# Optimization experiments

Hardware: AMD Instinct MI355X
Metric: run time of the kernel (lower is better)

The kernel has to match this reference:

```python
import jax, jax.numpy as jnp
import numpy as np

H, D, KV, S, PAST, BS, NB = 32, 128, 8, 128, 8064, 128, 128
T = PAST + S          # total context = 8192
NBLK = T // BS        # logical blocks used = 64
NEG = jnp.float32(-1e30)


def setup_inputs() -> dict:
    key = jax.random.key(0)
    ks = jax.random.split(key, 6)
    q = jax.random.normal(ks[0], (1, H, S, D), jnp.float32)
    k = jax.random.normal(ks[1], (1, KV, S, D), jnp.float32)
    v = jax.random.normal(ks[2], (1, KV, S, D), jnp.float32)
    pk = jax.random.normal(ks[3], (NB, KV, BS, D), jnp.float32)
    pv = jax.random.normal(ks[4], (NB, KV, BS, D), jnp.float32)
    # block table: 64 logical blocks mapped to distinct physical blocks (paged indirection)
    bt = jax.random.permutation(ks[5], NB)[:NBLK].astype(jnp.int32)
    return dict(
        query_state=q, key_state=k, value_state=v,
        attn_mask=jnp.ones((1,), jnp.float32),  # unused: causal prefill path (use_attention_mask=False)
        past_key_state=pk, past_value_state=pv,
        seq_position=PAST,
        scale=jnp.float32(1.0 / np.sqrt(D)),
        block_tables=bt, block_size=BS,
    )


def reference(query_state, key_state, value_state, attn_mask,
              past_key_state, past_value_state, seq_position, scale,
              block_tables, block_size):
    # phase == 'prefill', use_attention_mask=False -> paged_causal_attn_prefill
    kvh = past_key_state.shape[1]
    s_new = query_state.shape[2]
    total = seq_position + s_new  # static python int

    # --- append new K/V into the paged cache at positions [seq_position, total) ---
    pos_new = seq_position + jnp.arange(s_new)
    blk = block_tables[pos_new // block_size]
    off = pos_new % block_size
    k_new = jnp.transpose(key_state[0], (1, 0, 2))    # [S, KV, D]
    v_new = jnp.transpose(value_state[0], (1, 0, 2))
    kc = past_key_state.at[blk, :, off, :].set(k_new)
    vc = past_value_state.at[blk, :, off, :].set(v_new)

    # --- gather the full context [0, total) through the block table ---
    pos = jnp.arange(total)
    blk_a = block_tables[pos // block_size]
    off_a = pos % block_size
    K = kc[blk_a, :, off_a, :]   # [T, KV, D]
    V = vc[blk_a, :, off_a, :]

    # --- grouped-query causal attention ---
    g = query_state.shape[1] // kvh
    q = query_state.reshape(kvh, g, s_new, -1)                 # [KV, G, S, D]
    scores = jnp.einsum('kgsd,tkd->kgst', q, K) * scale        # [KV, G, S, T]
    causal = pos[None, :] <= (seq_position + jnp.arange(s_new))[:, None]  # [S, T]
    scores = jnp.where(causal[None, None], scores, NEG)
    probs = jax.nn.softmax(scores, axis=-1)
    out = jnp.einsum('kgst,tkd->kgsd', probs, V)               # [KV, G, S, D]

    h = kvh * g
    out = out.reshape(1, h, s_new, -1)                         # [1, H, S, D]
    out = jnp.transpose(out, (0, 2, 1, 3)).reshape(1, s_new, h * out.shape[-1])
    return out
```

## Files before the change

kernel.cpp:

```cpp
#include <hip/hip_runtime.h>
#include <hip/hip_bf16.h>


typedef unsigned short u16;
typedef unsigned int u32;
typedef __bf16 bf16x8 __attribute__((ext_vector_type(8)));
typedef float f32x16 __attribute__((ext_vector_type(16)));
typedef float f32x4 __attribute__((ext_vector_type(4)));
typedef u32 u32x4 __attribute__((ext_vector_type(4)));
typedef u32 u32x2 __attribute__((ext_vector_type(2)));

#define NHEAD 32
#define DH 128
#define NKV 8
#define SQ 128
#define PAST_T 8064
#define TOTAL_T 8192
#define BK 32
#define KSTR 136
#define VSTR 34
#define WSPP (16384 + 256)
#define MSUB 17.3123405f

__device__ __forceinline__ u32 pk2f(float lo, float hi) {
  union {
    __hip_bfloat162 b;
    u32 u;
  } cv;
  cv.b = __float22bfloat162_rn(make_float2(lo, hi));
  return cv.u;
}

template <int NPART>
__global__ __launch_bounds__(512, 1) void flash_part(
    const float* __restrict__ q, const float* __restrict__ knew,
    const float* __restrict__ vnew, const float* __restrict__ pk,
    const float* __restrict__ pv, const int* __restrict__ btab,
    const float* __restrict__ scp, float* __restrict__ ws) {
  constexpr int CHUNK = TOTAL_T / NPART;
  constexpr int NITER = CHUNK / BK;
  __shared__ __attribute__((aligned(16))) u16 k_s[2 * BK * KSTR];
  __shared__ __attribute__((aligned(16))) u16 vt_s[2 * DH * VSTR];
  __shared__ int bt_s[64];

  const int bid = blockIdx.x;
  const int kv = bid & 7;
  const int t = bid >> 3;
  const int p = t % NPART;
  const int gp = t / NPART;

  const int tid = threadIdx.x;
  const int wid = tid >> 6;
  const int lane = tid & 63;
  const int g2 = wid & 1;
  const int w = wid >> 1;
  const int h = kv * 4 + gp * 2 + g2;
  const int l31 = lane & 31, grp = lane >> 5;
  const int pstart = p * CHUNK;

  if (tid < 64) bt_s[tid] = btab[tid];
  const float qs = scp[0] * 1.44269504f;

  u32x4 qf[8];
  {
    const float* qp = q + ((size_t)(h * SQ + w * 32 + l31)) * DH;
#pragma unroll
    for (int st = 0; st < 8; ++st) {
      const f32x4 a = *(const f32x4*)(qp + st * 16 + grp * 8);
      const f32x4 b = *(const f32x4*)(qp + st * 16 + grp * 8 + 4);
      u32x4 f;
      f[0] = pk2f(a[0] * qs, a[1] * qs);
      f[1] = pk2f(a[2] * qs, a[3] * qs);
      f[2] = pk2f(b[0] * qs, b[1] * qs);
      f[3] = pk2f(b[2] * qs, b[3] * qs);
      qf[st] = f;
    }
  }

  f32x16 oacc[4];
#pragma unroll
  for (int i = 0; i < 4; ++i)
#pragma unroll
    for (int rr = 0; rr < 16; ++rr) oacc[i][rr] = 0.0f;
  float l_acc = 0.0f;

  __syncthreads();

  f32x4 kr0, kr1, v0, v1;
  const int kc4 = (tid & 31) * 4;
  const int ktrow = tid >> 5;
  const int va4 = (tid & 31) * 4;
  const int vtp = tid >> 5;

  auto load_tile = [&](int it) {
    const int t0 = pstart + it * BK;
    const float *sk, *sv;
    if (t0 < PAST_T) {
      const size_t boff =
          (((size_t)bt_s[t0 >> 7] * NKV + kv) * 128 + (t0 & 127)) * (size_t)DH;
      sk = pk + boff;
      sv = pv + boff;
    } else {
      const size_t noff = ((size_t)kv * SQ + (t0 - PAST_T)) * (size_t)DH;
      sk = knew + noff;
      sv = vnew + noff;
    }
    kr0 = *(const f32x4*)(sk + (size_t)ktrow * DH + kc4);
    kr1 = *(const f32x4*)(sk + (size_t)(ktrow + 16) * DH + kc4);
    v0 = *(const f32x4*)(sv + (size_t)(2 * vtp) * DH + va4);
    v1 = *(const f32x4*)(sv + (size_t)(2 * vtp + 1) * DH + va4);
  };
  auto store_tile = [&](int buf) {
    u16* ks = k_s + buf * (BK * KSTR);
    u16* vs = vt_s + buf * (DH * VSTR);
    {
      u32x2 pw;
      pw[0] = pk2f(kr0[0], kr0[1]);
      pw[1] = pk2f(kr0[2], kr0[3]);
      *(u32x2*)&ks[ktrow * KSTR + kc4] = pw;
    }
    {
      u32x2 pw;
      pw[0] = pk2f(kr1[0], kr1[1]);
      pw[1] = pk2f(kr1[2], kr1[3]);
      *(u32x2*)&ks[(ktrow + 16) * KSTR + kc4] = pw;
    }
#pragma unroll
    for (int j = 0; j < 4; ++j)
      *(u32*)&vs[(va4 + j) * VSTR + 2 * vtp] = pk2f(v0[j], v1[j]);
  };

  load_tile(0);
  store_tile(0);
  __syncthreads();

  for (int it = 0; it < NITER; ++it) {
    const int buf = it & 1;
    if (it + 1 < NITER) load_tile(it + 1);

    const u16* ks = k_s + buf * (BK * KSTR);
    const u16* vs = vt_s + buf * (DH * VSTR);
    const int t0 = pstart + it * BK;

    f32x16 sacc;
#pragma unroll
    for (int rr = 0; rr < 16; ++rr) sacc[rr] = 0.0f;
#pragma unroll
    for (int st = 0; st < 8; ++st) {
      const u32x4 kf = *(const u32x4*)&ks[l31 * KSTR + st * 16 + grp * 8];
      sacc = __builtin_amdgcn_mfma_f32_32x32x16_bf16(
          __builtin_bit_cast(bf16x8, kf), __builtin_bit_cast(bf16x8, qf[st]),
          sacc, 0, 0, 0);
    }

    const int qcol = w * 32 + l31;
    float pr[16];
    if (t0 > PAST_T - BK) {
#pragma unroll
      for (int rr = 0; rr < 16; ++rr) {
        const int trow = (rr & 3) + 8 * (rr >> 2) + 4 * grp;
        const float e = exp2f(sacc[rr] - MSUB);
        pr[rr] = ((t0 + trow - PAST_T) > qcol) ? 0.0f : e;
      }
    } else {
#pragma unroll
      for (int rr = 0; rr < 16; ++rr) pr[rr] = exp2f(sacc[rr] - MSUB);
    }
    float rs = 0.0f;
#pragma unroll
    for (int rr = 0; rr < 16; ++rr) rs += pr[rr];
    l_acc += rs;

    u32 pkk[8], xch[8];
#pragma unroll
    for (int j = 0; j < 8; ++j) pkk[j] = pk2f(pr[2 * j], pr[2 * j + 1]);
#pragma unroll
    for (int j = 0; j < 8; ++j) xch[j] = (u32)__shfl_xor((int)pkk[j], 32, 64);

    u32x4 pf1, pf2;
    pf1[0] = grp ? xch[2] : pkk[0];
    pf1[1] = grp ? xch[3] : pkk[1];
    pf1[2] = grp ? pkk[2] : xch[0];
    pf1[3] = grp ? pkk[3] : xch[1];
    pf2[0] = grp ? xch[6] : pkk[4];
    pf2[1] = grp ? xch[7] : pkk[5];
    pf2[2] = grp ? pkk[6] : xch[4];
    pf2[3] = grp ? pkk[7] : xch[5];

#pragma unroll
    for (int dt = 0; dt < 4; ++dt) {
      const int dd = dt * 32 + l31;
      const u16* vp = &vs[dd * VSTR + grp * 8];
      u32x4 av;
      av[0] = *(const u32*)(vp + 0);
      av[1] = *(const u32*)(vp + 2);
      av[2] = *(const u32*)(vp + 4);
      av[3] = *(const u32*)(vp + 6);
      oacc[dt] = __builtin_amdgcn_mfma_f32_32x32x16_bf16(
          __builtin_bit_cast(bf16x8, av), __builtin_bit_cast(bf16x8, pf1),
          oacc[dt], 0, 0, 0);
      const u16* vq = vp + 16;
      u32x4 bv;
      bv[0] = *(const u32*)(vq + 0);
      bv[1] = *(const u32*)(vq + 2);
      bv[2] = *(const u32*)(vq + 4);
      bv[3] = *(const u32*)(vq + 6);
      oacc[dt] = __builtin_amdgcn_mfma_f32_32x32x16_bf16(
          __builtin_bit_cast(bf16x8, bv), __builtin_bit_cast(bf16x8, pf2),
          oacc[dt], 0, 0, 0);
    }

    if (it + 1 < NITER) store_tile(buf ^ 1);
    __syncthreads();
  }

  float* wsp = ws + (size_t)(h * NPART + p) * WSPP;
#pragma unroll
  for (int dt = 0; dt < 4; ++dt)
#pragma unroll
    for (int rr = 0; rr < 16; ++rr) {
      const int dd = dt * 32 + (rr & 3) + 8 * (rr >> 2) + 4 * grp;
      wsp[dd * 128 + w * 32 + l31] = oacc[dt][rr];
    }
  const float l_tot = l_acc + __shfl_xor(l_acc, 32, 64);
  if (grp == 0) wsp[16384 + w * 32 + l31] = l_tot;
}

template <int NPART>
__global__ __launch_bounds__(256, 2) void combine_out(
    const float* __restrict__ ws, float* __restrict__ out) {
  __shared__ float rden_s[128];
  __shared__ float tr_s[128 * 9];

  const int dblk = blockIdx.x;
  const int h = blockIdx.y;
  const int tid = threadIdx.x;
  const float* base = ws + (size_t)h * NPART * WSPP;

  if (tid < 128) {
    float denom = 0.0f;
#pragma unroll
    for (int pp = 0; pp < NPART; ++pp)
      denom += base[(size_t)pp * WSPP + 16384 + tid];
    rden_s[tid] = 1.0f / denom;
  }
  __syncthreads();

  const int sq = tid & 31, dr = tid >> 5;
  {
    const int d = dblk * 8 + dr;
    float a[4] = {0.0f, 0.0f, 0.0f, 0.0f};
#pragma unroll
    for (int pp = 0; pp < NPART; ++pp) {
      const f32x4 o = *(const f32x4*)&base[(size_t)pp * WSPP + d * 128 + sq * 4];
#pragma unroll
      for (int j = 0; j < 4; ++j) a[j] += o[j];
    }
#pragma unroll
    for (int j = 0; j < 4; ++j)
      tr_s[(sq * 4 + j) * 9 + dr] = a[j] * rden_s[sq * 4 + j];
  }
  __syncthreads();

  {
    const int s = tid >> 1, dl0 = (tid & 1) * 4;
    f32x4 o;
#pragma unroll
    for (int j = 0; j < 4; ++j) o[j] = tr_s[s * 9 + dl0 + j];
    *(f32x4*)(out + (size_t)s * (NHEAD * DH) + h * DH + dblk * 8 + dl0) = o;
  }
}

extern "C" void kernel_launch(void* const* d_in, const int* in_sizes, int n_in,
                              void* d_out, int out_size, void* d_ws,
                              size_t ws_size, hipStream_t stream) {
  const float* q = (const float*)d_in[0];
  const float* knew = (const float*)d_in[1];
  const float* vnew = (const float*)d_in[2];
  const float* pk = (const float*)d_in[4];
  const float* pv = (const float*)d_in[5];
  const float* scp = (const float*)d_in[7];
  const int* btab = (const int*)d_in[8];
  float* ws = (float*)d_ws;
  float* out = (float*)d_out;

  const size_t need16 = (size_t)NHEAD * 16 * WSPP * sizeof(float);
  const size_t need8 = (size_t)NHEAD * 8 * WSPP * sizeof(float);
  if (ws_size >= need16) {
    flash_part<16><<<dim3(8 * 2 * 16), 512, 0, stream>>>(q, knew, vnew, pk, pv,
                                                         btab, scp, ws);
    combine_out<16><<<dim3(16, NHEAD), 256, 0, stream>>>(ws, out);
  } else if (ws_size >= need8) {
    flash_part<8><<<dim3(8 * 2 * 8), 512, 0, stream>>>(q, knew, vnew, pk, pv,
                                                       btab, scp, ws);
    combine_out<8><<<dim3(16, NHEAD), 256, 0, stream>>>(ws, out);
  }
}
```

Measured before the change: 172.6 us.

## Double key tile to 64 rows and use permlane32 swap for P exchange

Raises the per-iteration key/value tile from 32 to 64 tokens. Each iteration now runs two independent score MFMA chains and two P·V passes, which halves the number of barriers and loop iterations and gives more loads in flight per prefetch. It also replaces the shuffle-xor plus select exchange of packed probabilities with the permlane32_swap builtin when that builtin is available. The cost is more registers and double the LDS for staging, and NITER/partition boundaries must remain divisible by the larger tile.

```diff
diff --git a/kernel.cpp b/kernel.cpp
--- a/kernel.cpp
+++ b/kernel.cpp
@@ -9,6 +9,7 @@
 typedef float f32x4 __attribute__((ext_vector_type(4)));
 typedef u32 u32x4 __attribute__((ext_vector_type(4)));
 typedef u32 u32x2 __attribute__((ext_vector_type(2)));
+typedef int i32x2 __attribute__((ext_vector_type(2)));
 
 #define NHEAD 32
 #define DH 128
@@ -16,9 +17,9 @@
 #define SQ 128
 #define PAST_T 8064
 #define TOTAL_T 8192
-#define BK 32
+#define BK 64
 #define KSTR 136
-#define VSTR 34
+#define VSTR 66
 #define WSPP (16384 + 256)
 #define MSUB 17.3123405f
 
@@ -86,7 +87,7 @@
 
   __syncthreads();
 
-  f32x4 kr0, kr1, v0, v1;
+  f32x4 kr0, kr1, kr2, kr3, v0, v1, v2, v3;
   const int kc4 = (tid & 31) * 4;
   const int ktrow = tid >> 5;
   const int va4 = (tid & 31) * 4;
@@ -105,10 +106,14 @@
       sk = knew + noff;
       sv = vnew + noff;
     }
-    kr0 = *(const f32x4*)(sk + (size_t)ktrow * DH + kc4);
+    kr0 = *(const f32x4*)(sk + (size_t)(ktrow + 0) * DH + kc4);
     kr1 = *(const f32x4*)(sk + (size_t)(ktrow + 16) * DH + kc4);
+    kr2 = *(const f32x4*)(sk + (size_t)(ktrow + 32) * DH + kc4);
+    kr3 = *(const f32x4*)(sk + (size_t)(ktrow + 48) * DH + kc4);
     v0 = *(const f32x4*)(sv + (size_t)(2 * vtp) * DH + va4);
     v1 = *(const f32x4*)(sv + (size_t)(2 * vtp + 1) * DH + va4);
+    v2 = *(const f32x4*)(sv + (size_t)(2 * vtp + 32) * DH + va4);
+    v3 = *(const f32x4*)(sv + (size_t)(2 * vtp + 33) * DH + va4);
   };
   auto store_tile = [&](int buf) {
     u16* ks = k_s + buf * (BK * KSTR);
@@ -117,7 +122,7 @@
       u32x2 pw;
       pw[0] = pk2f(kr0[0], kr0[1]);
       pw[1] = pk2f(kr0[2], kr0[3]);
-      *(u32x2*)&ks[ktrow * KSTR + kc4] = pw;
+      *(u32x2*)&ks[(ktrow + 0) * KSTR + kc4] = pw;
     }
     {
       u32x2 pw;
@@ -125,9 +130,23 @@
       pw[1] = pk2f(kr1[2], kr1[3]);
       *(u32x2*)&ks[(ktrow + 16) * KSTR + kc4] = pw;
     }
-#pragma unroll
-    for (int j = 0; j < 4; ++j)
+    {
+      u32x2 pw;
+      pw[0] = pk2f(kr2[0], kr2[1]);
+      pw[1] = pk2f(kr2[2], kr2[3]);
+      *(u32x2*)&ks[(ktrow + 32) * KSTR + kc4] = pw;
+    }
+    {
+      u32x2 pw;
+      pw[0] = pk2f(kr3[0], kr3[1]);
+      pw[1] = pk2f(kr3[2], kr3[3]);
+      *(u32x2*)&ks[(ktrow + 48) * KSTR + kc4] = pw;
+    }
+#pragma unroll
+    for (int j = 0; j < 4; ++j) {
       *(u32*)&vs[(va4 + j) * VSTR + 2 * vtp] = pk2f(v0[j], v1[j]);
+      *(u32*)&vs[(va4 + j) * VSTR + 2 * vtp + 32] = pk2f(v2[j], v3[j]);
+    }
   };
 
   load_tile(0);
@@ -141,73 +160,111 @@
     const u16* ks = k_s + buf * (BK * KSTR);
     const u16* vs = vt_s + buf * (DH * VSTR);
     const int t0 = pstart + it * BK;
-
-    f32x16 sacc;
-#pragma unroll
-    for (int rr = 0; rr < 16; ++rr) sacc[rr] = 0.0f;
+    const int qcol = w * 32 + l31;
+
+    f32x16 sacc0, sacc1;
+#pragma unroll
+    for (int rr = 0; rr < 16; ++rr) sacc0[rr] = 0.0f;
+#pragma unroll
+    for (int rr = 0; rr < 16; ++rr) sacc1[rr] = 0.0f;
 #pragma unroll
     for (int st = 0; st < 8; ++st) {
-      const u32x4 kf = *(const u32x4*)&ks[l31 * KSTR + st * 16 + grp * 8];
-      sacc = __builtin_amdgcn_mfma_f32_32x32x16_bf16(
-          __builtin_bit_cast(bf16x8, kf), __builtin_bit_cast(bf16x8, qf[st]),
-          sacc, 0, 0, 0);
-    }
-
-    const int qcol = w * 32 + l31;
-    float pr[16];
-    if (t0 > PAST_T - BK) {
-#pragma unroll
-      for (int rr = 0; rr < 16; ++rr) {
-        const int trow = (rr & 3) + 8 * (rr >> 2) + 4 * grp;
-        const float e = exp2f(sacc[rr] - MSUB);
-        pr[rr] = ((t0 + trow - PAST_T) > qcol) ? 0.0f : e;
+      const u32x4 kf0 = *(const u32x4*)&ks[l31 * KSTR + st * 16 + grp * 8];
+      sacc0 = __builtin_amdgcn_mfma_f32_32x32x16_bf16(
+          __builtin_bit_cast(bf16x8, kf0), __builtin_bit_cast(bf16x8, qf[st]),
+          sacc0, 0, 0, 0);
+      const u32x4 kf1 =
+          *(const u32x4*)&ks[(l31 + 32) * KSTR + st * 16 + grp * 8];
+      sacc1 = __builtin_amdgcn_mfma_f32_32x32x16_bf16(
+          __builtin_bit_cast(bf16x8, kf1), __builtin_bit_cast(bf16x8, qf[st]),
+          sacc1, 0, 0, 0);
+    }
+
+#pragma unroll
+    for (int ts = 0; ts < 2; ++ts) {
+      const f32x16& sacc = ts ? sacc1 : sacc0;
+      const int tb = t0 + ts * 32;
+
+      float pr[16];
+      if (tb > PAST_T - 32) {
+#pragma unroll
+        for (int rr = 0; rr < 16; ++rr) {
+          const int trow = (rr & 3) + 8 * (rr >> 2) + 4 * grp;
+          const float e = exp2f(sacc[rr] - MSUB);
+          pr[rr] = ((tb + trow - PAST_T) > qcol) ? 0.0f : e;
+        }
+      } else {
+#pragma unroll
+        for (int rr = 0; rr < 16; ++rr) pr[rr] = exp2f(sacc[rr] - MSUB);
       }
-    } else {
-#pragma unroll
-      for (int rr = 0; rr < 16; ++rr) pr[rr] = exp2f(sacc[rr] - MSUB);
-    }
-    float rs = 0.0f;
-#pragma unroll
-    for (int rr = 0; rr < 16; ++rr) rs += pr[rr];
-    l_acc += rs;
-
-    u32 pkk[8], xch[8];
-#pragma unroll
-    for (int j = 0; j < 8; ++j) pkk[j] = pk2f(pr[2 * j], pr[2 * j + 1]);
-#pragma unroll
-    for (int j = 0; j < 8; ++j) xch[j] = (u32)__shfl_xor((int)pkk[j], 32, 64);
-
-    u32x4 pf1, pf2;
-    pf1[0] = grp ? xch[2] : pkk[0];
-    pf1[1] = grp ? xch[3] : pkk[1];
-    pf1[2] = grp ? pkk[2] : xch[0];
-    pf1[3] = grp ? pkk[3] : xch[1];
-    pf2[0] = grp ? xch[6] : pkk[4];
-    pf2[1] = grp ? xch[7] : pkk[5];
-    pf2[2] = grp ? pkk[6] : xch[4];
-    pf2[3] = grp ? pkk[7] : xch[5];
-
-#pragma unroll
-    for (int dt = 0; dt < 4; ++dt) {
-      const int dd = dt * 32 + l31;
-      const u16* vp = &vs[dd * VSTR + grp * 8];
-      u32x4 av;
-      av[0] = *(const u32*)(vp + 0);
-      av[1] = *(const u32*)(vp + 2);
-      av[2] = *(const u32*)(vp + 4);
-      av[3] = *(const u32*)(vp + 6);
-      oacc[dt] = __builtin_amdgcn_mfma_f32_32x32x16_bf16(
-          __builtin_bit_cast(bf16x8, av), __builtin_bit_cast(bf16x8, pf1),
-          oacc[dt], 0, 0, 0);
-      const u16* vq = vp + 16;
-      u32x4 bv;
-      bv[0] = *(const u32*)(vq + 0);
-      bv[1] = *(const u32*)(vq + 2);
-      bv[2] = *(const u32*)(vq + 4);
-      bv[3] = *(const u32*)(vq + 6);
-      oacc[dt] = __builtin_amdgcn_mfma_f32_32x32x16_bf16(
-          __builtin_bit_cast(bf16x8, bv), __builtin_bit_cast(bf16x8, pf2),
-          oacc[dt], 0, 0, 0);
+      float rs = 0.0f;
+#pragma unroll
+      for (int rr = 0; rr < 16; ++rr) rs += pr[rr];
+      l_acc += rs;
+
+      u32 pkk[8];
+#pragma unroll
+      for (int j = 0; j < 8; ++j) pkk[j] = pk2f(pr[2 * j], pr[2 * j + 1]);
+
+      u32x4 pf1, pf2;
+#if __has_builtin(__builtin_amdgcn_permlane32_swap)
+      {
+        const i32x2 s02 = __builtin_amdgcn_permlane32_swap(
+            (int)pkk[0], (int)pkk[2], false, false);
+        const i32x2 s13 = __builtin_amdgcn_permlane32_swap(
+            (int)pkk[1], (int)pkk[3], false, false);
+        const i32x2 s46 = __builtin_amdgcn_permlane32_swap(
+            (int)pkk[4], (int)pkk[6], false, false);
+        const i32x2 s57 = __builtin_amdgcn_permlane32_swap(
+            (int)pkk[5], (int)pkk[7], false, false);
+        pf1[0] = (u32)s02[0];
+        pf1[1] = (u32)s13[0];
+        pf1[2] = (u32)s02[1];
+        pf1[3] = (u32)s13[1];
+        pf2[0] = (u32)s46[0];
+        pf2[1] = (u32)s57[0];
+        pf2[2] = (u32)s46[1];
+        pf2[3] = (u32)s57[1];
+      }
+#else
+      {
+        u32 xch[8];
+#pragma unroll
+        for (int j = 0; j < 8; ++j)
+          xch[j] = (u32)__shfl_xor((int)pkk[j], 32, 64);
+        pf1[0] = grp ? xch[2] : pkk[0];
+        pf1[1] = grp ? xch[3] : pkk[1];
+        pf1[2] = grp ? pkk[2] : xch[0];
+        pf1[3] = grp ? pkk[3] : xch[1];
+        pf2[0] = grp ? xch[6] : pkk[4];
+        pf2[1] = grp ? xch[7] : pkk[5];
+        pf2[2] = grp ? pkk[6] : xch[4];
+        pf2[3] = grp ? pkk[7] : xch[5];
+      }
+#endif
+
+#pragma unroll
+      for (int dt = 0; dt < 4; ++dt) {
+        const int dd = dt * 32 + l31;
+        const u16* vp = &vs[dd * VSTR + ts * 32 + grp * 8];
+        u32x4 av;
+        av[0] = *(const u32*)(vp + 0);
+        av[1] = *(const u32*)(vp + 2);
+        av[2] = *(const u32*)(vp + 4);
+        av[3] = *(const u32*)(vp + 6);
+        oacc[dt] = __builtin_amdgcn_mfma_f32_32x32x16_bf16(
+            __builtin_bit_cast(bf16x8, av), __builtin_bit_cast(bf16x8, pf1),
+            oacc[dt], 0, 0, 0);
+        const u16* vq = vp + 16;
+        u32x4 bv;
+        bv[0] = *(const u32*)(vq + 0);
+        bv[1] = *(const u32*)(vq + 2);
+        bv[2] = *(const u32*)(vq + 4);
+        bv[3] = *(const u32*)(vq + 6);
+        oacc[dt] = __builtin_amdgcn_mfma_f32_32x32x16_bf16(
+            __builtin_bit_cast(bf16x8, bv), __builtin_bit_cast(bf16x8, pf2),
+            oacc[dt], 0, 0, 0);
+      }
     }
 
     if (it + 1 < NITER) store_tile(buf ^ 1);
```

Result: no change. 170.2 us (-1.4%).
